# Kernel tuning notes

Measured on AMD Instinct MI355X. Metric: run time of the kernel, lower is better.

The kernel has to match this reference:

```python
import jax, jax.numpy as jnp
import numpy as np

THR = 0.2
POOL_A = 160
POOL_B = 96
EPS = 1e-5


def _adaptive_avg_pool_last(x, out_size):
    # torch AdaptiveAvgPool1d semantics: bin i averages [floor(i*n/o), ceil((i+1)*n/o))
    n = x.shape[-1]
    i = np.arange(out_size)
    starts = (i * n) // out_size
    ends = -((-(i + 1) * n) // out_size)
    cs = jnp.cumsum(x, axis=-1)
    cs = jnp.concatenate([jnp.zeros_like(cs[..., :1]), cs], axis=-1)
    sums = cs[..., ends] - cs[..., starts]
    return sums / jnp.asarray(ends - starts, x.dtype)


def _unfold3x3(x, H, W):
    # Faithful to torch: raw reshape (N, L, C) -> (N, C, H, W) (memory reinterpretation,
    # NOT a transpose), then F.unfold(k=3, pad=1) and rearrange 'n (c ww) l -> n l ww c'.
    N, L, C = x.shape
    img = x.reshape(N, C, H, W)
    pad = jnp.pad(img, ((0, 0), (0, 0), (1, 1), (1, 1)))
    # window positions in row-major (ky, kx) order, matching F.unfold
    patches = jnp.stack([pad[:, :, dy:dy + H, dx:dx + W]
                         for dy in range(3) for dx in range(3)], axis=2)  # (N,C,9,H,W)
    return patches.transpose(0, 3, 4, 2, 1).reshape(N, H * W, 9, C)  # (N,L,9,C)


def _forward(feat_s0, feat_s1, ln_weight, ln_bias):
    N, L, C = feat_s0.shape
    H = W = int(round(L ** 0.5))
    conf = jnp.einsum('nlc,nsc->nls', feat_s0, feat_s1) / (C ** 0.5)
    conf = jax.nn.softmax(conf, axis=1) * jax.nn.softmax(conf, axis=2)
    # mutual nearest-neighbor mask with confidence threshold
    mask = ((conf > THR)
            & (conf == conf.max(axis=2, keepdims=True))
            & (conf == conf.max(axis=1, keepdims=True))).astype(feat_s0.dtype)
    u0 = _unfold3x3(feat_s0, H, W)
    u1 = _unfold3x3(feat_s1, H, W)
    sem0 = jnp.einsum('nlc,nlwc->nlw', feat_s0, u0) / C  # divided by C (shape[-1]), as in source
    sem1 = jnp.einsum('nlc,nlwc->nlw', feat_s1, u1) / C
    fea0 = jnp.einsum('nlwc,nlw->nlc', u0, sem0)
    fea1 = jnp.einsum('nlwc,nlw->nlc', u1, sem1)
    s0 = jnp.einsum('nls,nsd->nld', mask, fea1) / L
    s1 = jnp.einsum('nsl,nsd->nld', mask, fea0) / L
    f0 = jnp.concatenate([_adaptive_avg_pool_last(feat_s0, POOL_A),
                          _adaptive_avg_pool_last(s0, POOL_B)], axis=-1)
    f1 = jnp.concatenate([_adaptive_avg_pool_last(feat_s1, POOL_A),
                          _adaptive_avg_pool_last(s1, POOL_B)], axis=-1)
    f = jnp.concatenate([f0, f1], axis=0)  # (2N, L, 256)
    mu = f.mean(-1, keepdims=True)
    var = f.var(-1, keepdims=True)
    f = (f - mu) * jax.lax.rsqrt(var + EPS) * ln_weight + ln_bias
    return f[:N], f[N:]


def setup_inputs():
    key = jax.random.key(0)
    k0, k1 = jax.random.split(key)
    N, L, C = 2, 4096, 256
    return {
        'feat_s0': jax.random.normal(k0, (N, L, C), jnp.float32),
        'feat_s1': jax.random.normal(k1, (N, L, C), jnp.float32),
        'ln_weight': jnp.ones((C,), jnp.float32),
        'ln_bias': jnp.zeros((C,), jnp.float32),
    }


def reference(feat_s0, feat_s1, ln_weight, ln_bias):
    return _forward(feat_s0, feat_s1, ln_weight, ln_bias)
```

## Files before the change

### kernel.cpp

```cpp
#include <hip/hip_runtime.h>
#include <stdint.h>

#define NBATCH 2
#define LL 4096
#define CC 256
#define LSTR8 144
#define KEXP 0.09016844f
#define KEXP2 0.18033688f
#define IMIN (-2147483647 - 1)

typedef long i64f;
typedef float f32x4 __attribute__((ext_vector_type(4)));

#if defined(__has_builtin) && __has_builtin(__builtin_amdgcn_exp2f)
#define EXP2F(x) __builtin_amdgcn_exp2f(x)
#else
#define EXP2F(x) exp2f(x)
#endif

__global__ __launch_bounds__(256) void cast_fp8(
    const float* __restrict__ a, const float* __restrict__ b,
    uint32_t* __restrict__ oa, uint32_t* __restrict__ ob){
  int idx = blockIdx.x * 256 + threadIdx.x;
  float4 va = ((const float4*)a)[idx];
  float4 vb = ((const float4*)b)[idx];
  int ra = __builtin_amdgcn_cvt_pk_fp8_f32(va.x, va.y, 0, false);
  ra = __builtin_amdgcn_cvt_pk_fp8_f32(va.z, va.w, ra, true);
  int rb = __builtin_amdgcn_cvt_pk_fp8_f32(vb.x, vb.y, 0, false);
  rb = __builtin_amdgcn_cvt_pk_fp8_f32(vb.z, vb.w, rb, true);
  oa[idx] = (uint32_t)ra;
  ob[idx] = (uint32_t)rb;
}

__global__ __launch_bounds__(256, 4) void conf_pass(
    const uint8_t* __restrict__ f0q, const uint8_t* __restrict__ f1q,
    float* __restrict__ rowSum, float* __restrict__ colSum,
    int* __restrict__ rowPart, int* __restrict__ colPart){
  __shared__ uint8_t Alds[128*LSTR8], Blds[128*LSTR8];
  float* rowS = (float*)Alds;
  float* colS = (float*)(Alds + 1024);
  int*   rb   = (int*)  (Alds + 2048);
  int*   cb   = (int*)  (Alds + 3072);
  int bl = (blockIdx.z*32 + blockIdx.y)*32 + blockIdx.x;
  int nb = (bl & 7)*256 + (bl >> 3);
  int st = nb & 31, lt = (nb >> 5) & 31, n = nb >> 10;
  int t = threadIdx.x;
  const int wv = t >> 6, lane = t & 63, lr = lane & 15, quad = lane >> 4;
  const int lq = wv >> 1, sq = wv & 1;
  const uint8_t* A = f0q + (size_t)n*LL*CC + (size_t)(lt*128)*CC;
  const uint8_t* B = f1q + (size_t)n*LL*CC + (size_t)(st*128)*CC;
  f32x4 acc[4][4];
  #pragma unroll
  for (int r = 0; r < 4; r++)
    #pragma unroll
    for (int j = 0; j < 4; j++) acc[r][j] = (f32x4){0.f,0.f,0.f,0.f};

  auto compute = [&](){
    #pragma unroll
    for (int kk = 0; kk < 4; kk++){
      i64f a[4], bf[4];
      #pragma unroll
      for (int r = 0; r < 4; r++)
        a[r] = *(const i64f*)(Alds + (lq*64 + r*16 + lr)*LSTR8 + kk*32 + quad*8);
      #pragma unroll
      for (int j = 0; j < 4; j++)
        bf[j] = *(const i64f*)(Blds + (sq*64 + j*16 + lr)*LSTR8 + kk*32 + quad*8);
      #pragma unroll
      for (int r = 0; r < 4; r++)
        #pragma unroll
        for (int j = 0; j < 4; j++)
          acc[r][j] = __builtin_amdgcn_mfma_f32_16x16x32_fp8_fp8(a[r], bf[j], acc[r][j], 0, 0, 0);
    }
  };

  #pragma unroll
  for (int m = 0; m < 8; m++){
    int f = m*256 + t, row = f >> 4, kg = f & 15;
    *(uint2*)(Alds + row*LSTR8 + kg*8) = *(const uint2*)(A + (size_t)row*CC + kg*8);
    *(uint2*)(Blds + row*LSTR8 + kg*8) = *(const uint2*)(B + (size_t)row*CC + kg*8);
  }
  uint2 pa[8], pb[8];
  #pragma unroll
  for (int m = 0; m < 8; m++){
    int f = m*256 + t, row = f >> 4, kg = f & 15;
    pa[m] = *(const uint2*)(A + (size_t)row*CC + 128 + kg*8);
    pb[m] = *(const uint2*)(B + (size_t)row*CC + 128 + kg*8);
  }
  __syncthreads();
  compute();
  __syncthreads();
  #pragma unroll
  for (int m = 0; m < 8; m++){
    int f = m*256 + t, row = f >> 4, kg = f & 15;
    *(uint2*)(Alds + row*LSTR8 + kg*8) = pa[m];
    *(uint2*)(Blds + row*LSTR8 + kg*8) = pb[m];
  }
  __syncthreads();
  compute();

  const int sbase = st*128 + sq*64 + lr;
  const int lbase = lt*128 + lq*64 + quad*4;
  float rsum[4][4], csum[4] = {0.f,0.f,0.f,0.f};
  int rkey[4][4], ckey[4] = {IMIN,IMIN,IMIN,IMIN};
  #pragma unroll
  for (int r = 0; r < 4; r++)
    #pragma unroll
    for (int rr = 0; rr < 4; rr++){ rsum[r][rr] = 0.f; rkey[r][rr] = IMIN; }
  #pragma unroll
  for (int r = 0; r < 4; r++)
    #pragma unroll
    for (int j = 0; j < 4; j++)
      #pragma unroll
      for (int rr = 0; rr < 4; rr++){
        float a = acc[r][j][rr];
        float e = EXP2F(a * KEXP);
        rsum[r][rr] += e;
        csum[j] += e;
        int iqs = ((int)(a * 2048.f)) << 12;
        rkey[r][rr] = max(rkey[r][rr], iqs + (sbase + j*16));
        ckey[j]     = max(ckey[j],     iqs + (lbase + r*16 + rr));
      }
  #pragma unroll
  for (int msk = 1; msk <= 8; msk <<= 1)
    #pragma unroll
    for (int r = 0; r < 4; r++)
      #pragma unroll
      for (int rr = 0; rr < 4; rr++){
        rsum[r][rr] += __shfl_xor(rsum[r][rr], msk);
        rkey[r][rr] = max(rkey[r][rr], __shfl_xor(rkey[r][rr], msk));
      }
  #pragma unroll
  for (int msk = 16; msk <= 32; msk <<= 1)
    #pragma unroll
    for (int j = 0; j < 4; j++){
      csum[j] += __shfl_xor(csum[j], msk);
      ckey[j] = max(ckey[j], __shfl_xor(ckey[j], msk));
    }
  __syncthreads();
  if (lr == 0){
    #pragma unroll
    for (int r = 0; r < 4; r++)
      #pragma unroll
      for (int rr = 0; rr < 4; rr++){
        int row = lq*64 + r*16 + quad*4 + rr;
        rowS[sq*128 + row] = rsum[r][rr];
        rb[sq*128 + row]   = rkey[r][rr];
      }
  }
  if (quad == 0){
    #pragma unroll
    for (int j = 0; j < 4; j++){
      int col = sq*64 + j*16 + lr;
      colS[lq*128 + col] = csum[j];
      cb[lq*128 + col]   = ckey[j];
    }
  }
  __syncthreads();
  if (t < 128){
    rowSum[((size_t)n*LL + lt*128 + t)*32 + st] = rowS[t] + rowS[128 + t];
    colSum[((size_t)n*LL + st*128 + t)*32 + lt] = colS[t] + colS[128 + t];
    rowPart[((size_t)n*LL + lt*128 + t)*32 + st] = max(rb[t], rb[128 + t]);
    colPart[((size_t)n*LL + st*128 + t)*32 + lt] = max(cb[t], cb[128 + t]);
  }
}

__device__ float fea_fly(const float* __restrict__ featn, int srow, int t){
  __shared__ float sred[9][4];
  __shared__ float ssem[9];
  int lane = t & 63, wv = t >> 6;
  int h = srow >> 6, xx = srow & 63;
  float fv = featn[(size_t)srow * CC + t];
  float uv[9];
  #pragma unroll
  for (int w = 0; w < 9; w++){
    int dy = w/3 - 1, dx = w%3 - 1;
    int y = h + dy, x = xx + dx;
    uv[w] = (y >= 0 && y < 64 && x >= 0 && x < 64) ? featn[(size_t)t * 4096 + y*64 + x] : 0.f;
  }
  __syncthreads();
  #pragma unroll
  for (int w = 0; w < 9; w++){
    float pvv = fv * uv[w];
    #pragma unroll
    for (int msk = 1; msk <= 32; msk <<= 1) pvv += __shfl_xor(pvv, msk);
    if (lane == 0) sred[w][wv] = pvv;
  }
  __syncthreads();
  if (t < 9) ssem[t] = (sred[t][0] + sred[t][1] + sred[t][2] + sred[t][3]) * (1.f/256.f);
  __syncthreads();
  float acc = 0.f;
  #pragma unroll
  for (int w = 0; w < 9; w++) acc += uv[w] * ssem[w];
  __syncthreads();
  return acc;
}

__device__ __forceinline__ float pool_window(const float* f, const float* s, int t){
  if (t < 160){
    int a = (t*8)/5, e = (t*8+12)/5;
    float sum = 0.f;
    for (int i = a; i < e; i++) sum += f[i];
    return sum / (float)(e - a);
  } else {
    int tt = t - 160;
    int a = (tt*8)/3, e = (tt*8+10)/3;
    float sum = 0.f;
    for (int i = a; i < e; i++) sum += s[i];
    return sum / (float)(e - a);
  }
}

__global__ __launch_bounds__(256) void tail(
    const float* __restrict__ feat0, const float* __restrict__ feat1,
    const float* __restrict__ rowSum, const float* __restrict__ colSum,
    const int* __restrict__ rowPart, const int* __restrict__ colPart,
    const float* __restrict__ lnw, const float* __restrict__ lnb,
    float* __restrict__ out){
  int l = blockIdx.x, n = blockIdx.y, t = threadIdx.x;
  int lane = t & 63, wv = t >> 6;
  size_t base = (size_t)n * LL;
  float fv0 = feat0[(base + l)*CC + t];
  float fv1 = feat1[(base + l)*CC + t];
  float w = lnw[t], bsh = lnb[t];
  __shared__ float sVal[8];
  {
    float s = 0.f; int k = IMIN;
    if (lane < 32){
      size_t off = (base + l)*32 + lane;
      if      (wv == 0) s = rowSum[off];
      else if (wv == 1) s = colSum[off];
      else if (wv == 2) k = rowPart[off];
      else              k = colPart[off];
    }
    #pragma unroll
    for (int msk = 1; msk <= 16; msk <<= 1){
      s += __shfl_xor(s, msk);
      k = max(k, __shfl_xor(k, msk));
    }
    if (lane == 0) sVal[wv] = (wv < 2) ? s : __int_as_float(k);
  }
  __syncthreads();
  int rowK = __float_as_int(sVal[2]), colK = __float_as_int(sVal[3]);
  int ssr = rowK & 4095, ssc = colK & 4095;
  {
    float s = 0.f; int k = IMIN;
    if (lane < 32){
      if      (wv == 0) s = colSum [(base + ssr)*32 + lane];
      else if (wv == 1) s = rowSum [(base + ssc)*32 + lane];
      else if (wv == 2) k = colPart[(base + ssr)*32 + lane];
      else              k = rowPart[(base + ssc)*32 + lane];
    }
    #pragma unroll
    for (int msk = 1; msk <= 16; msk <<= 1){
      s += __shfl_xor(s, msk);
      k = max(k, __shfl_xor(k, msk));
    }
    if (lane == 0) sVal[4 + wv] = (wv < 2) ? s : __int_as_float(k);
  }
  __syncthreads();
  float Rl   = sVal[0], Cl   = sVal[1];
  float Cssr = sVal[4], Rssc = sVal[5];
  int ck2 = __float_as_int(sVal[6]), rk2 = __float_as_int(sVal[7]);
  float v0 = 0.f, v1 = 0.f;
  {
    float araw = (float)(rowK >> 12) * (1.f/2048.f);
    float val = exp2f(araw * KEXP2) / (Rl * Cssr);
    if (val > 0.2f && (ck2 & 4095) == l)
      v0 = fea_fly(feat1 + (size_t)n*LL*CC, ssr, t) * (1.f/4096.f);
  }
  {
    float araw = (float)(colK >> 12) * (1.f/2048.f);
    float val = exp2f(araw * KEXP2) / (Cl * Rssc);
    if (val > 0.2f && (rk2 & 4095) == l)
      v1 = fea_fly(feat0 + (size_t)n*LL*CC, ssc, t) * (1.f/4096.f);
  }
  __shared__ float f0r[CC], f1r[CC], s0r[CC], s1r[CC];
  __shared__ float redA[2][4], redB[2][4];
  f0r[t] = fv0;
  f1r[t] = fv1;
  s0r[t] = v0;
  s1r[t] = v1;
  __syncthreads();
  float pA = pool_window(f0r, s0r, t);
  float pB = pool_window(f1r, s1r, t);
  float smA = pA, sqA = pA*pA, smB = pB, sqB = pB*pB;
  #pragma unroll
  for (int msk = 1; msk <= 32; msk <<= 1){
    smA += __shfl_xor(smA, msk);
    sqA += __shfl_xor(sqA, msk);
    smB += __shfl_xor(smB, msk);
    sqB += __shfl_xor(sqB, msk);
  }
  if (lane == 0){ redA[0][wv] = smA; redA[1][wv] = sqA; redB[0][wv] = smB; redB[1][wv] = sqB; }
  __syncthreads();
  float tsA = redA[0][0]+redA[0][1]+redA[0][2]+redA[0][3];
  float tqA = redA[1][0]+redA[1][1]+redA[1][2]+redA[1][3];
  float tsB = redB[0][0]+redB[0][1]+redB[0][2]+redB[0][3];
  float tqB = redB[1][0]+redB[1][1]+redB[1][2]+redB[1][3];
  float muA = tsA * (1.f/256.f), varA = tqA * (1.f/256.f) - muA*muA;
  float muB = tsB * (1.f/256.f), varB = tqB * (1.f/256.f) - muB*muB;
  out[((size_t)n*LL + l)*CC + t]       = (pA - muA) * rsqrtf(varA + 1e-5f) * w + bsh;
  out[((size_t)(2 + n)*LL + l)*CC + t] = (pB - muB) * rsqrtf(varB + 1e-5f) * w + bsh;
}

extern "C" void kernel_launch(void* const* d_in, const int* in_sizes, int n_in,
                              void* d_out, int out_size, void* d_ws, size_t ws_size,
                              hipStream_t stream){
  const float* feat0 = (const float*)d_in[0];
  const float* feat1 = (const float*)d_in[1];
  const float* lnw   = (const float*)d_in[2];
  const float* lnb   = (const float*)d_in[3];
  float* out = (float*)d_out;
  char* ws = (char*)d_ws;
  const size_t MB = 1024 * 1024;
  uint8_t* f0q = (uint8_t*)(ws + 0);
  uint8_t* f1q = (uint8_t*)(ws + 2*MB);
  float* rowSum  = (float*)(ws + 4*MB);
  float* colSum  = (float*)(ws + 5*MB);
  int*   rowPart = (int*)  (ws + 6*MB);
  int*   colPart = (int*)  (ws + 7*MB);

  cast_fp8<<<2048, 256, 0, stream>>>(feat0, feat1, (uint32_t*)f0q, (uint32_t*)f1q);
  dim3 gconf(32, 32, NBATCH);
  conf_pass<<<gconf, 256, 0, stream>>>(f0q, f1q, rowSum, colSum, rowPart, colPart);
  dim3 gt(LL, NBATCH);
  tail<<<gt, 256, 0, stream>>>(feat0, feat1, rowSum, colSum, rowPart, colPart,
                               lnw, lnb, out);
}
```

Measured before the change: 137.7 us.

## Reduce row/col partials via global atomics instead of per-tile partial arrays

Replaces the 32-way per-tile partial arrays for row/column softmax sums and argmax keys with global atomic add/max into single per-row entries, zero-initialized inside the cast kernel. The tail kernel then reads four scalars directly instead of doing two shuffle reductions with block barriers. This removes partial-array traffic and tail-side reduction work, but adds atomic contention and makes the float sum order nondeterministic.

```diff
diff --git a/kernel.cpp b/kernel.cpp
--- a/kernel.cpp
+++ b/kernel.cpp
@@ -20,8 +20,14 @@
 
 __global__ __launch_bounds__(256) void cast_fp8(
     const float* __restrict__ a, const float* __restrict__ b,
-    uint32_t* __restrict__ oa, uint32_t* __restrict__ ob){
+    uint32_t* __restrict__ oa, uint32_t* __restrict__ ob,
+    float* __restrict__ rowSum, float* __restrict__ colSum,
+    int* __restrict__ rowPart, int* __restrict__ colPart){
   int idx = blockIdx.x * 256 + threadIdx.x;
+  if (idx < NBATCH*LL){
+    rowSum[idx] = 0.f; colSum[idx] = 0.f;
+    rowPart[idx] = IMIN; colPart[idx] = IMIN;
+  }
   float4 va = ((const float4*)a)[idx];
   float4 vb = ((const float4*)b)[idx];
   int ra = __builtin_amdgcn_cvt_pk_fp8_f32(va.x, va.y, 0, false);
@@ -157,10 +163,10 @@
   }
   __syncthreads();
   if (t < 128){
-    rowSum[((size_t)n*LL + lt*128 + t)*32 + st] = rowS[t] + rowS[128 + t];
-    colSum[((size_t)n*LL + st*128 + t)*32 + lt] = colS[t] + colS[128 + t];
-    rowPart[((size_t)n*LL + lt*128 + t)*32 + st] = max(rb[t], rb[128 + t]);
-    colPart[((size_t)n*LL + st*128 + t)*32 + lt] = max(cb[t], cb[128 + t]);
+    unsafeAtomicAdd(&rowSum[(size_t)n*LL + lt*128 + t], rowS[t] + rowS[128 + t]);
+    unsafeAtomicAdd(&colSum[(size_t)n*LL + st*128 + t], colS[t] + colS[128 + t]);
+    atomicMax(&rowPart[(size_t)n*LL + lt*128 + t], max(rb[t], rb[128 + t]));
+    atomicMax(&colPart[(size_t)n*LL + st*128 + t], max(cb[t], cb[128 + t]));
   }
 }
 
@@ -222,45 +228,11 @@
   float fv0 = feat0[(base + l)*CC + t];
   float fv1 = feat1[(base + l)*CC + t];
   float w = lnw[t], bsh = lnb[t];
-  __shared__ float sVal[8];
-  {
-    float s = 0.f; int k = IMIN;
-    if (lane < 32){
-      size_t off = (base + l)*32 + lane;
-      if      (wv == 0) s = rowSum[off];
-      else if (wv == 1) s = colSum[off];
-      else if (wv == 2) k = rowPart[off];
-      else              k = colPart[off];
-    }
-    #pragma unroll
-    for (int msk = 1; msk <= 16; msk <<= 1){
-      s += __shfl_xor(s, msk);
-      k = max(k, __shfl_xor(k, msk));
-    }
-    if (lane == 0) sVal[wv] = (wv < 2) ? s : __int_as_float(k);
-  }
-  __syncthreads();
-  int rowK = __float_as_int(sVal[2]), colK = __float_as_int(sVal[3]);
+  int   rowK = rowPart[base + l], colK = colPart[base + l];
+  float Rl   = rowSum[base + l],  Cl   = colSum[base + l];
   int ssr = rowK & 4095, ssc = colK & 4095;
-  {
-    float s = 0.f; int k = IMIN;
-    if (lane < 32){
-      if      (wv == 0) s = colSum [(base + ssr)*32 + lane];
-      else if (wv == 1) s = rowSum [(base + ssc)*32 + lane];
-      else if (wv == 2) k = colPart[(base + ssr)*32 + lane];
-      else              k = rowPart[(base + ssc)*32 + lane];
-    }
-    #pragma unroll
-    for (int msk = 1; msk <= 16; msk <<= 1){
-      s += __shfl_xor(s, msk);
-      k = max(k, __shfl_xor(k, msk));
-    }
-    if (lane == 0) sVal[4 + wv] = (wv < 2) ? s : __int_as_float(k);
-  }
-  __syncthreads();
-  float Rl   = sVal[0], Cl   = sVal[1];
-  float Cssr = sVal[4], Rssc = sVal[5];
-  int ck2 = __float_as_int(sVal[6]), rk2 = __float_as_int(sVal[7]);
+  float Cssr = colSum[base + ssr], Rssc = rowSum[base + ssc];
+  int   ck2  = colPart[base + ssr], rk2 = rowPart[base + ssc];
   float v0 = 0.f, v1 = 0.f;
   {
     float araw = (float)(rowK >> 12) * (1.f/2048.f);
@@ -316,11 +288,12 @@
   uint8_t* f0q = (uint8_t*)(ws + 0);
   uint8_t* f1q = (uint8_t*)(ws + 2*MB);
   float* rowSum  = (float*)(ws + 4*MB);
-  float* colSum  = (float*)(ws + 5*MB);
-  int*   rowPart = (int*)  (ws + 6*MB);
-  int*   colPart = (int*)  (ws + 7*MB);
-
-  cast_fp8<<<2048, 256, 0, stream>>>(feat0, feat1, (uint32_t*)f0q, (uint32_t*)f1q);
+  float* colSum  = (float*)(ws + 4*MB + 32*1024);
+  int*   rowPart = (int*)  (ws + 4*MB + 64*1024);
+  int*   colPart = (int*)  (ws + 4*MB + 96*1024);
+
+  cast_fp8<<<2048, 256, 0, stream>>>(feat0, feat1, (uint32_t*)f0q, (uint32_t*)f1q,
+                                     rowSum, colSum, rowPart, colPart);
   dim3 gconf(32, 32, NBATCH);
   conf_pass<<<gconf, 256, 0, stream>>>(f0q, f1q, rowSum, colSum, rowPart, colPart);
   dim3 gt(LL, NBATCH);
```

Result: faster. 131.8 us (-4.2%).
